# Kernel optimization log

Hardware: AMD Instinct MI355X
Metric: run time of the kernel (lower is better)

## Reference

```python
import jax, jax.numpy as jnp
import numpy as np

N_EDGES = 4096
HIDDEN = 256
EDGE_DIM = 128
NUM_HEADS = 4
NUM_GRAPHS = 64


def setup_inputs() -> dict:
    key0 = jax.random.key(0)
    ks = jax.random.split(key0, 10)
    s = 0.02
    inp = {
        "query": jax.random.normal(ks[0], (N_EDGES, HIDDEN), jnp.float32),
        "key": jax.random.normal(ks[1], (N_EDGES, EDGE_DIM), jnp.float32),
        "value": jax.random.normal(ks[2], (N_EDGES, EDGE_DIM), jnp.float32),
        "edge_graph_index": jnp.sort(
            jax.random.randint(ks[3], (N_EDGES,), 0, NUM_GRAPHS)
        ),
        # edge_proj: Linear(edge_context_dim -> hidden_dim)
        "w_edge": jax.random.normal(ks[4], (HIDDEN, EDGE_DIM), jnp.float32) * s,
        "b_edge": jnp.zeros((HIDDEN,), jnp.float32),
        # nn.MultiheadAttention packed in-projection [3H, H] and bias [3H]
        "w_in": jax.random.normal(ks[5], (3 * HIDDEN, HIDDEN), jnp.float32) * s,
        "b_in": jnp.zeros((3 * HIDDEN,), jnp.float32),
        # out_proj: Linear(hidden -> hidden)
        "w_out": jax.random.normal(ks[6], (HIDDEN, HIDDEN), jnp.float32) * s,
        "b_out": jnp.zeros((HIDDEN,), jnp.float32),
    }
    return inp


def reference(query, key, value, edge_graph_index,
              w_edge, b_edge, w_in, b_in, w_out, b_out):
    # Segment-wise cross attention == block-diagonal masked attention over all edges.
    N, H = query.shape
    nh = NUM_HEADS
    dh = H // nh

    # edge feature projection (applied to both key and value, as in the module)
    K = key @ w_edge.T + b_edge      # [N, H]
    V = value @ w_edge.T + b_edge    # [N, H]

    wq, wk, wv = jnp.split(w_in, 3, axis=0)
    bq, bk, bv = jnp.split(b_in, 3)
    Qh = (query @ wq.T + bq).reshape(N, nh, dh)
    Kh = (K @ wk.T + bk).reshape(N, nh, dh)
    Vh = (V @ wv.T + bv).reshape(N, nh, dh)

    scale = 1.0 / jnp.sqrt(jnp.asarray(dh, query.dtype))
    scores = jnp.einsum("nhd,mhd->hnm", Qh, Kh) * scale  # [nh, N, N]

    # attention only within the same graph segment
    same_graph = edge_graph_index[:, None] == edge_graph_index[None, :]  # [N, N]
    neg = jnp.finfo(scores.dtype).min
    scores = jnp.where(same_graph[None, :, :], scores, neg)

    attn = jax.nn.softmax(scores, axis=-1)                 # [nh, N, N]
    out = jnp.einsum("hnm,mhd->nhd", attn, Vh).reshape(N, H)
    out = out @ w_out.T + b_out
    return query + out
```

## Files before the change

kernel.cpp:

```cpp
#include <hip/hip_runtime.h>

#define N_EDGES 4096
#define HIDDEN  256
#define EDGE_DIM 128
#define NUM_HEADS 4
#define NUM_GRAPHS 64
#define DH 64

typedef __attribute__((ext_vector_type(8))) short short8;
typedef __attribute__((ext_vector_type(4))) float f32x4;

__device__ __forceinline__ unsigned short f2bf(float f) {
  unsigned u = __builtin_bit_cast(unsigned, f);
  u += 0x7FFF + ((u >> 16) & 1);
  return (unsigned short)(u >> 16);
}
__device__ __forceinline__ float bf2f(unsigned short u) {
  return __builtin_bit_cast(float, (unsigned)u << 16);
}
__device__ __forceinline__ short8 cvt8(float4 x, float4 y) {
  short8 v;
  v[0] = (short)f2bf(x.x); v[1] = (short)f2bf(x.y);
  v[2] = (short)f2bf(x.z); v[3] = (short)f2bf(x.w);
  v[4] = (short)f2bf(y.x); v[5] = (short)f2bf(y.y);
  v[6] = (short)f2bf(y.z); v[7] = (short)f2bf(y.w);
  return v;
}
__device__ __forceinline__ float4 us4f(ushort4 v) {
  float4 f;
  f.x = bf2f(v.x); f.y = bf2f(v.y); f.z = bf2f(v.z); f.w = bf2f(v.w);
  return f;
}

__device__ __forceinline__ int lbound(const int* __restrict__ a, int n, int v) {
  int lo = 0, hi = n;
  while (lo < hi) { int mid = (lo + hi) >> 1; if (a[mid] < v) lo = mid + 1; else hi = mid; }
  return lo;
}

template<bool ABF, bool OUTF32>
__device__ __forceinline__ void gemm_core(const void* Ap, const float* W,
                                          const float* bias, const float* res,
                                          void* Cp, const int K) {
  const int t = threadIdx.x;
  const int m0 = blockIdx.x * 64, n0 = blockIdx.y * 64;
  __shared__ unsigned short As[64 * 40];
  __shared__ unsigned short Ws[64 * 40];
  const int r = t >> 2, kg = t & 3;
  const int lane = t & 63, w = t >> 6;
  const int quad = lane >> 4, l16 = lane & 15;
  const int wm = (w >> 1) * 32, wn = (w & 1) * 32;
  f32x4 acc[2][2] = {};
  const float* pw = W + (size_t)(n0 + r) * K + kg * 8;
  float4 w0 = *(const float4*)(pw), w1 = *(const float4*)(pw + 4);
  const unsigned short* pa16 = (const unsigned short*)Ap + (size_t)(m0 + r) * K + kg * 8;
  const float* pa32 = (const float*)Ap + (size_t)(m0 + r) * K + kg * 8;
  short8 a16; float4 a0, a1;
  if (ABF) a16 = *(const short8*)pa16;
  else { a0 = *(const float4*)pa32; a1 = *(const float4*)(pa32 + 4); }
  for (int kc = 0; kc < K; kc += 32) {
    short8 na16; float4 na0, na1, nw0, nw1;
    if (kc + 32 < K) {
      if (ABF) na16 = *(const short8*)(pa16 + kc + 32);
      else { na0 = *(const float4*)(pa32 + kc + 32); na1 = *(const float4*)(pa32 + kc + 36); }
      nw0 = *(const float4*)(pw + kc + 32); nw1 = *(const float4*)(pw + kc + 36);
    }
    __syncthreads();
    short8 av = ABF ? a16 : cvt8(a0, a1);
    *(short8*)&As[r * 40 + kg * 8] = av;
    *(short8*)&Ws[r * 40 + kg * 8] = cvt8(w0, w1);
    __syncthreads();
    short8 af0 = *(const short8*)&As[(wm + l16) * 40 + quad * 8];
    short8 af1 = *(const short8*)&As[(wm + 16 + l16) * 40 + quad * 8];
    short8 bf0 = *(const short8*)&Ws[(wn + l16) * 40 + quad * 8];
    short8 bf1 = *(const short8*)&Ws[(wn + 16 + l16) * 40 + quad * 8];
    acc[0][0] = __builtin_amdgcn_mfma_f32_16x16x32_bf16(af0, bf0, acc[0][0], 0, 0, 0);
    acc[0][1] = __builtin_amdgcn_mfma_f32_16x16x32_bf16(af0, bf1, acc[0][1], 0, 0, 0);
    acc[1][0] = __builtin_amdgcn_mfma_f32_16x16x32_bf16(af1, bf0, acc[1][0], 0, 0, 0);
    acc[1][1] = __builtin_amdgcn_mfma_f32_16x16x32_bf16(af1, bf1, acc[1][1], 0, 0, 0);
    a16 = na16; a0 = na0; a1 = na1; w0 = nw0; w1 = nw1;
  }
#pragma unroll
  for (int j = 0; j < 2; ++j) {
    const int col = n0 + wn + j * 16 + l16;
    const float bj = bias[col];
#pragma unroll
    for (int i = 0; i < 2; ++i) {
#pragma unroll
      for (int reg = 0; reg < 4; ++reg) {
        const int row = m0 + wm + i * 16 + quad * 4 + reg;
        const size_t idx = (size_t)row * HIDDEN + col;
        float v = acc[i][j][reg] + bj;
        if (OUTF32) ((float*)Cp)[idx] = v + res[idx];
        else        ((unsigned short*)Cp)[idx] = f2bf(v);
      }
    }
  }
}

__global__ __launch_bounds__(256) void proj1(const float* __restrict__ query,
                                             const float* __restrict__ key,
                                             const float* __restrict__ value,
                                             const float* __restrict__ w_in,
                                             const float* __restrict__ b_in,
                                             const float* __restrict__ w_edge,
                                             const float* __restrict__ b_edge,
                                             const int* __restrict__ gidx,
                                             unsigned short* Qh, unsigned short* Ek,
                                             unsigned short* Ev, int* segStart) {
  if (blockIdx.z == 0 && blockIdx.x == 0 && blockIdx.y == 0 && threadIdx.x <= NUM_GRAPHS)
    segStart[threadIdx.x] = lbound(gidx, N_EDGES, threadIdx.x);
  if (blockIdx.z == 0)      gemm_core<false, false>(query, w_in,   b_in,   nullptr, Qh, 256);
  else if (blockIdx.z == 1) gemm_core<false, false>(key,   w_edge, b_edge, nullptr, Ek, 128);
  else                      gemm_core<false, false>(value, w_edge, b_edge, nullptr, Ev, 128);
}

__global__ __launch_bounds__(256) void proj2(const unsigned short* __restrict__ Ek,
                                             const unsigned short* __restrict__ Ev,
                                             const float* __restrict__ w_in,
                                             const float* __restrict__ b_in,
                                             unsigned short* Kh, unsigned short* Vh) {
  if (blockIdx.z == 0) gemm_core<true, false>(Ek, w_in + 256 * HIDDEN, b_in + 256, nullptr, Kh, 256);
  else                 gemm_core<true, false>(Ev, w_in + 512 * HIDDEN, b_in + 512, nullptr, Vh, 256);
}

__global__ __launch_bounds__(256) void attn_segment(const unsigned short* __restrict__ Qh,
                                                    const unsigned short* __restrict__ Kh,
                                                    const unsigned short* __restrict__ Vh,
                                                    const int* __restrict__ segStart,
                                                    unsigned short* __restrict__ ao) {
  const int graph = blockIdx.x, h = blockIdx.y, zg = blockIdx.z;
  const int segLo = segStart[graph];
  const int segHi = segStart[graph + 1];
  const int segLen = segHi - segLo;
  const int t = threadIdx.x, lane = t & 63, w = t >> 6;
  __shared__ float Qs[16][68], Ks[64][68], Vs[64][68];
  __shared__ float Ps[4][64][4];
  const float scale = 0.125f;
  const int r0 = w * 4;

  for (int chunk = zg; chunk * 16 < segLen; chunk += 8) {
    const int row0 = segLo + chunk * 16;
    const int rows = min(16, segHi - row0);
    __syncthreads();
    { int r = t >> 4, d4 = (t & 15) * 4;
      if (r < rows)
        *(float4*)&Qs[r][d4] =
            us4f(*(const ushort4*)(Qh + (size_t)(row0 + r) * HIDDEN + h * DH + d4)); }

    float accv[4] = {0.f, 0.f, 0.f, 0.f}, lsum[4] = {0.f, 0.f, 0.f, 0.f};

    for (int c0 = segLo; c0 < segHi; c0 += 64) {
      const int tc = min(64, segHi - c0);
      __syncthreads();
#pragma unroll
      for (int it = 0; it < 4; ++it) {
        int s = t + it * 256; int j = s >> 4; int d4 = (s & 15) * 4;
        if (j < tc) {
          *(float4*)&Ks[j][d4] =
              us4f(*(const ushort4*)(Kh + (size_t)(c0 + j) * HIDDEN + h * DH + d4));
          *(float4*)&Vs[j][d4] =
              us4f(*(const ushort4*)(Vh + (size_t)(c0 + j) * HIDDEN + h * DH + d4));
        }
      }
      __syncthreads();
      float4 kreg[16];
#pragma unroll
      for (int d4 = 0; d4 < 16; ++d4) kreg[d4] = *(const float4*)&Ks[lane][d4 * 4];
      float p[4];
#pragma unroll
      for (int r = 0; r < 4; ++r) {
        float s = 0.f;
#pragma unroll
        for (int d4 = 0; d4 < 16; ++d4) {
          float4 q = *(const float4*)&Qs[r0 + r][d4 * 4];
          s += q.x * kreg[d4].x + q.y * kreg[d4].y + q.z * kreg[d4].z + q.w * kreg[d4].w;
        }
        p[r] = (lane < tc && r0 + r < rows) ? __expf(s * scale) : 0.f;
        lsum[r] += p[r];
      }
      float4 p4; p4.x = p[0]; p4.y = p[1]; p4.z = p[2]; p4.w = p[3];
      *(float4*)&Ps[w][lane][0] = p4;
      __asm__ volatile("s_waitcnt lgkmcnt(0)" ::: "memory");
      for (int j = 0; j < tc; ++j) {
        const float v = Vs[j][lane];
        float4 pj = *(const float4*)&Ps[w][j][0];
        accv[0] += pj.x * v; accv[1] += pj.y * v;
        accv[2] += pj.z * v; accv[3] += pj.w * v;
      }
    }
#pragma unroll
    for (int off = 32; off; off >>= 1)
#pragma unroll
      for (int r = 0; r < 4; ++r) lsum[r] += __shfl_xor(lsum[r], off);
#pragma unroll
    for (int r = 0; r < 4; ++r)
      if (r0 + r < rows)
        ao[(size_t)(row0 + r0 + r) * HIDDEN + h * DH + lane] = f2bf(accv[r] / lsum[r]);
  }
}

__global__ __launch_bounds__(256) void outproj(const unsigned short* __restrict__ ao,
                                               const float* __restrict__ w_out,
                                               const float* __restrict__ b_out,
                                               const float* __restrict__ query,
                                               float* __restrict__ out) {
  gemm_core<true, true>(ao, w_out, b_out, query, out, 256);
}

extern "C" void kernel_launch(void* const* d_in, const int* in_sizes, int n_in,
                              void* d_out, int out_size, void* d_ws, size_t ws_size,
                              hipStream_t stream) {
  const float* query  = (const float*)d_in[0];
  const float* key    = (const float*)d_in[1];
  const float* value  = (const float*)d_in[2];
  const int*   gidx   = (const int*)d_in[3];
  const float* w_edge = (const float*)d_in[4];
  const float* b_edge = (const float*)d_in[5];
  const float* w_in   = (const float*)d_in[6];
  const float* b_in   = (const float*)d_in[7];
  const float* w_out  = (const float*)d_in[8];
  const float* b_out  = (const float*)d_in[9];
  float* out = (float*)d_out;

  int* segStart = (int*)d_ws;
  unsigned short* Qh = (unsigned short*)((char*)d_ws + 512);
  unsigned short* Ek = Qh + (size_t)N_EDGES * HIDDEN;
  unsigned short* Ev = Ek + (size_t)N_EDGES * HIDDEN;
  unsigned short* Kh = Ev + (size_t)N_EDGES * HIDDEN;
  unsigned short* Vh = Kh + (size_t)N_EDGES * HIDDEN;
  unsigned short* ao = Vh + (size_t)N_EDGES * HIDDEN;

  proj1<<<dim3(64, 4, 3), 256, 0, stream>>>(query, key, value, w_in, b_in,
                                            w_edge, b_edge, gidx, Qh, Ek, Ev, segStart);
  proj2<<<dim3(64, 4, 2), 256, 0, stream>>>(Ek, Ev, w_in, b_in, Kh, Vh);
  attn_segment<<<dim3(NUM_GRAPHS, NUM_HEADS, 8), 256, 0, stream>>>(Qh, Kh, Vh, segStart, ao);
  outproj<<<dim3(64, 4), 256, 0, stream>>>(ao, w_out, b_out, query, out);
}
```

Measured before the change: 117.7 us.

## Fold edge projection into K/V weights and fuse attention with output projection

Precomputes fused weights (w_in_k/v times w_edge) and biases in a small kernel, so key/value projection becomes one GEMM instead of two chained GEMMs with bf16 intermediates. Attention now loops over all heads inside a block and immediately applies the output projection plus residual using MFMA, eliminating the separate outproj kernel and the attention output buffer. This reduces launches and global traffic but cuts attention grid parallelism by the head count and reloads w_out from global per row chunk. Segment bounds are computed per block by binary search instead of a prepass.

```diff
diff --git a/kernel.cpp b/kernel.cpp
--- a/kernel.cpp
+++ b/kernel.cpp
@@ -38,174 +38,265 @@
   return lo;
 }
 
-template<bool ABF, bool OUTF32>
-__device__ __forceinline__ void gemm_core(const void* Ap, const float* W,
-                                          const float* bias, const float* res,
-                                          void* Cp, const int K) {
+template<bool WBF>
+__device__ __forceinline__ void gemm_tile(const float* __restrict__ Ap, const void* Wp,
+                                          const float* __restrict__ bias,
+                                          unsigned short* __restrict__ Cp, const int K,
+                                          const int m0, const int n0,
+                                          unsigned short* As, unsigned short* Ws) {
   const int t = threadIdx.x;
-  const int m0 = blockIdx.x * 64, n0 = blockIdx.y * 64;
-  __shared__ unsigned short As[64 * 40];
-  __shared__ unsigned short Ws[64 * 40];
   const int r = t >> 2, kg = t & 3;
   const int lane = t & 63, w = t >> 6;
   const int quad = lane >> 4, l16 = lane & 15;
   const int wm = (w >> 1) * 32, wn = (w & 1) * 32;
   f32x4 acc[2][2] = {};
-  const float* pw = W + (size_t)(n0 + r) * K + kg * 8;
-  float4 w0 = *(const float4*)(pw), w1 = *(const float4*)(pw + 4);
-  const unsigned short* pa16 = (const unsigned short*)Ap + (size_t)(m0 + r) * K + kg * 8;
-  const float* pa32 = (const float*)Ap + (size_t)(m0 + r) * K + kg * 8;
-  short8 a16; float4 a0, a1;
-  if (ABF) a16 = *(const short8*)pa16;
-  else { a0 = *(const float4*)pa32; a1 = *(const float4*)(pa32 + 4); }
+  const float* pa32 = Ap + (size_t)(m0 + r) * K + kg * 8;
+  const float*          pw32 = (const float*)Wp          + (size_t)(n0 + r) * K + kg * 8;
+  const unsigned short* pw16 = (const unsigned short*)Wp + (size_t)(n0 + r) * K + kg * 8;
+  short8 w16; float4 a0, a1, w0, w1;
+  a0 = *(const float4*)pa32; a1 = *(const float4*)(pa32 + 4);
+  if (WBF) w16 = *(const short8*)pw16;
+  else { w0 = *(const float4*)pw32; w1 = *(const float4*)(pw32 + 4); }
   for (int kc = 0; kc < K; kc += 32) {
-    short8 na16; float4 na0, na1, nw0, nw1;
+    short8 nw16; float4 na0, na1, nw0, nw1;
     if (kc + 32 < K) {
-      if (ABF) na16 = *(const short8*)(pa16 + kc + 32);
-      else { na0 = *(const float4*)(pa32 + kc + 32); na1 = *(const float4*)(pa32 + kc + 36); }
-      nw0 = *(const float4*)(pw + kc + 32); nw1 = *(const float4*)(pw + kc + 36);
+      na0 = *(const float4*)(pa32 + kc + 32); na1 = *(const float4*)(pa32 + kc + 36);
+      if (WBF) nw16 = *(const short8*)(pw16 + kc + 32);
+      else { nw0 = *(const float4*)(pw32 + kc + 32); nw1 = *(const float4*)(pw32 + kc + 36); }
     }
     __syncthreads();
-    short8 av = ABF ? a16 : cvt8(a0, a1);
-    *(short8*)&As[r * 40 + kg * 8] = av;
-    *(short8*)&Ws[r * 40 + kg * 8] = cvt8(w0, w1);
+    *(short8*)&As[r * 40 + kg * 8] = cvt8(a0, a1);
+    *(short8*)&Ws[r * 40 + kg * 8] = WBF ? w16 : cvt8(w0, w1);
     __syncthreads();
     short8 af0 = *(const short8*)&As[(wm + l16) * 40 + quad * 8];
     short8 af1 = *(const short8*)&As[(wm + 16 + l16) * 40 + quad * 8];
-    short8 bf0 = *(const short8*)&Ws[(wn + l16) * 40 + quad * 8];
-    short8 bf1 = *(const short8*)&Ws[(wn + 16 + l16) * 40 + quad * 8];
-    acc[0][0] = __builtin_amdgcn_mfma_f32_16x16x32_bf16(af0, bf0, acc[0][0], 0, 0, 0);
-    acc[0][1] = __builtin_amdgcn_mfma_f32_16x16x32_bf16(af0, bf1, acc[0][1], 0, 0, 0);
-    acc[1][0] = __builtin_amdgcn_mfma_f32_16x16x32_bf16(af1, bf0, acc[1][0], 0, 0, 0);
-    acc[1][1] = __builtin_amdgcn_mfma_f32_16x16x32_bf16(af1, bf1, acc[1][1], 0, 0, 0);
-    a16 = na16; a0 = na0; a1 = na1; w0 = nw0; w1 = nw1;
+    short8 bq0 = *(const short8*)&Ws[(wn + l16) * 40 + quad * 8];
+    short8 bq1 = *(const short8*)&Ws[(wn + 16 + l16) * 40 + quad * 8];
+    acc[0][0] = __builtin_amdgcn_mfma_f32_16x16x32_bf16(af0, bq0, acc[0][0], 0, 0, 0);
+    acc[0][1] = __builtin_amdgcn_mfma_f32_16x16x32_bf16(af0, bq1, acc[0][1], 0, 0, 0);
+    acc[1][0] = __builtin_amdgcn_mfma_f32_16x16x32_bf16(af1, bq0, acc[1][0], 0, 0, 0);
+    acc[1][1] = __builtin_amdgcn_mfma_f32_16x16x32_bf16(af1, bq1, acc[1][1], 0, 0, 0);
+    a0 = na0; a1 = na1; w16 = nw16; w0 = nw0; w1 = nw1;
   }
 #pragma unroll
   for (int j = 0; j < 2; ++j) {
     const int col = n0 + wn + j * 16 + l16;
     const float bj = bias[col];
 #pragma unroll
-    for (int i = 0; i < 2; ++i) {
+    for (int i = 0; i < 2; ++i)
 #pragma unroll
       for (int reg = 0; reg < 4; ++reg) {
         const int row = m0 + wm + i * 16 + quad * 4 + reg;
-        const size_t idx = (size_t)row * HIDDEN + col;
-        float v = acc[i][j][reg] + bj;
-        if (OUTF32) ((float*)Cp)[idx] = v + res[idx];
-        else        ((unsigned short*)Cp)[idx] = f2bf(v);
-      }
+        Cp[(size_t)row * HIDDEN + col] = f2bf(acc[i][j][reg] + bj);
+      }
+  }
+}
+
+__device__ __forceinline__ void wf_part(int bb, const float* __restrict__ w_in,
+                                        const float* __restrict__ b_in,
+                                        const float* __restrict__ w_edge,
+                                        const float* __restrict__ b_edge,
+                                        unsigned short* __restrict__ Wfk,
+                                        unsigned short* __restrict__ Wfv,
+                                        float* __restrict__ bfk, float* __restrict__ bfv,
+                                        unsigned short* As, unsigned short* Bs) {
+  const int sel = bb >> 3;
+  const int tt  = bb & 7;
+  const int n0  = (tt >> 1) * 64;
+  const int k0  = (tt & 1) * 64;
+  const float* Wp = w_in + (size_t)(256 + 256 * sel) * HIDDEN;
+  const float* bp = b_in + 256 + 256 * sel;
+  unsigned short* Wf = sel ? Wfv : Wfk;
+  float* bf = sel ? bfv : bfk;
+  const int t = threadIdx.x;
+  const int r = t >> 2, kg = t & 3;
+  const int lane = t & 63, w = t >> 6;
+  const int quad = lane >> 4, l16 = lane & 15;
+  const int wm = (w >> 1) * 32, wn = (w & 1) * 32;
+  if (k0 == 0) {
+    float s = 0.f;
+    const float* wrow = Wp + (size_t)(n0 + r) * HIDDEN + kg * 64;
+    const float* be = b_edge + kg * 64;
+#pragma unroll
+    for (int j = 0; j < 64; j += 4) {
+      float4 a = *(const float4*)(wrow + j);
+      float4 b = *(const float4*)(be + j);
+      s += a.x * b.x + a.y * b.y + a.z * b.z + a.w * b.w;
     }
-  }
-}
-
-__global__ __launch_bounds__(256) void proj1(const float* __restrict__ query,
-                                             const float* __restrict__ key,
-                                             const float* __restrict__ value,
-                                             const float* __restrict__ w_in,
-                                             const float* __restrict__ b_in,
-                                             const float* __restrict__ w_edge,
-                                             const float* __restrict__ b_edge,
-                                             const int* __restrict__ gidx,
-                                             unsigned short* Qh, unsigned short* Ek,
-                                             unsigned short* Ev, int* segStart) {
-  if (blockIdx.z == 0 && blockIdx.x == 0 && blockIdx.y == 0 && threadIdx.x <= NUM_GRAPHS)
-    segStart[threadIdx.x] = lbound(gidx, N_EDGES, threadIdx.x);
-  if (blockIdx.z == 0)      gemm_core<false, false>(query, w_in,   b_in,   nullptr, Qh, 256);
-  else if (blockIdx.z == 1) gemm_core<false, false>(key,   w_edge, b_edge, nullptr, Ek, 128);
-  else                      gemm_core<false, false>(value, w_edge, b_edge, nullptr, Ev, 128);
-}
-
-__global__ __launch_bounds__(256) void proj2(const unsigned short* __restrict__ Ek,
-                                             const unsigned short* __restrict__ Ev,
-                                             const float* __restrict__ w_in,
-                                             const float* __restrict__ b_in,
-                                             unsigned short* Kh, unsigned short* Vh) {
-  if (blockIdx.z == 0) gemm_core<true, false>(Ek, w_in + 256 * HIDDEN, b_in + 256, nullptr, Kh, 256);
-  else                 gemm_core<true, false>(Ev, w_in + 512 * HIDDEN, b_in + 512, nullptr, Vh, 256);
-}
-
-__global__ __launch_bounds__(256) void attn_segment(const unsigned short* __restrict__ Qh,
-                                                    const unsigned short* __restrict__ Kh,
-                                                    const unsigned short* __restrict__ Vh,
-                                                    const int* __restrict__ segStart,
-                                                    unsigned short* __restrict__ ao) {
-  const int graph = blockIdx.x, h = blockIdx.y, zg = blockIdx.z;
-  const int segLo = segStart[graph];
-  const int segHi = segStart[graph + 1];
+    s += __shfl_xor(s, 1); s += __shfl_xor(s, 2);
+    if (kg == 0) bf[n0 + r] = s + bp[n0 + r];
+  }
+  f32x4 facc[2][2] = {};
+  for (int j0 = 0; j0 < HIDDEN; j0 += 32) {
+    __syncthreads();
+    { const float* p = Wp + (size_t)(n0 + r) * HIDDEN + j0 + kg * 8;
+      float4 x0 = *(const float4*)p, x1 = *(const float4*)(p + 4);
+      *(short8*)&As[r * 40 + kg * 8] = cvt8(x0, x1); }
+    { const int j = t >> 3, k8 = (t & 7) * 8;
+      const float* p = w_edge + (size_t)(j0 + j) * EDGE_DIM + k0 + k8;
+      float4 b0 = *(const float4*)p, b1 = *(const float4*)(p + 4);
+      float bv[8] = {b0.x, b0.y, b0.z, b0.w, b1.x, b1.y, b1.z, b1.w};
+#pragma unroll
+      for (int i = 0; i < 8; ++i) Bs[(k8 + i) * 40 + j] = f2bf(bv[i]); }
+    __syncthreads();
+    short8 af0 = *(const short8*)&As[(wm + l16) * 40 + quad * 8];
+    short8 af1 = *(const short8*)&As[(wm + 16 + l16) * 40 + quad * 8];
+    short8 bq0 = *(const short8*)&Bs[(wn + l16) * 40 + quad * 8];
+    short8 bq1 = *(const short8*)&Bs[(wn + 16 + l16) * 40 + quad * 8];
+    facc[0][0] = __builtin_amdgcn_mfma_f32_16x16x32_bf16(af0, bq0, facc[0][0], 0, 0, 0);
+    facc[0][1] = __builtin_amdgcn_mfma_f32_16x16x32_bf16(af0, bq1, facc[0][1], 0, 0, 0);
+    facc[1][0] = __builtin_amdgcn_mfma_f32_16x16x32_bf16(af1, bq0, facc[1][0], 0, 0, 0);
+    facc[1][1] = __builtin_amdgcn_mfma_f32_16x16x32_bf16(af1, bq1, facc[1][1], 0, 0, 0);
+  }
+#pragma unroll
+  for (int jj = 0; jj < 2; ++jj)
+#pragma unroll
+    for (int ii = 0; ii < 2; ++ii)
+#pragma unroll
+      for (int reg = 0; reg < 4; ++reg) {
+        const int n = wm + ii * 16 + quad * 4 + reg;
+        const int k = wn + jj * 16 + l16;
+        Wf[(size_t)(n0 + n) * EDGE_DIM + k0 + k] = f2bf(facc[ii][jj][reg]);
+      }
+}
+
+__global__ __launch_bounds__(256) void k_wf(const float* __restrict__ w_in,
+                                            const float* __restrict__ b_in,
+                                            const float* __restrict__ w_edge,
+                                            const float* __restrict__ b_edge,
+                                            unsigned short* Wfk, unsigned short* Wfv,
+                                            float* bfk, float* bfv) {
+  __shared__ unsigned short As[64 * 40];
+  __shared__ unsigned short Bs[64 * 40];
+  wf_part(blockIdx.x, w_in, b_in, w_edge, b_edge, Wfk, Wfv, bfk, bfv, As, Bs);
+}
+
+__global__ __launch_bounds__(256) void k_proj(const float* __restrict__ query,
+                                              const float* __restrict__ key,
+                                              const float* __restrict__ value,
+                                              const float* __restrict__ w_in,
+                                              const float* __restrict__ b_in,
+                                              const unsigned short* __restrict__ Wfk,
+                                              const unsigned short* __restrict__ Wfv,
+                                              const float* __restrict__ bfk,
+                                              const float* __restrict__ bfv,
+                                              unsigned short* Qh, unsigned short* Kh,
+                                              unsigned short* Vh) {
+  __shared__ unsigned short As[64 * 40];
+  __shared__ unsigned short Ws[64 * 40];
+  const int m0 = blockIdx.x * 64, n0 = blockIdx.y * 64;
+  if (blockIdx.z == 0)      gemm_tile<false>(query, w_in, b_in, Qh, 256, m0, n0, As, Ws);
+  else if (blockIdx.z == 1) gemm_tile<true>(key, Wfk, bfk, Kh, 128, m0, n0, As, Ws);
+  else                      gemm_tile<true>(value, Wfv, bfv, Vh, 128, m0, n0, As, Ws);
+}
+
+__global__ __launch_bounds__(256) void k_attn_out(const unsigned short* __restrict__ Qh,
+                                                  const unsigned short* __restrict__ Kh,
+                                                  const unsigned short* __restrict__ Vh,
+                                                  const int* __restrict__ gidx,
+                                                  const float* __restrict__ w_out,
+                                                  const float* __restrict__ b_out,
+                                                  const float* __restrict__ query,
+                                                  float* __restrict__ out) {
+  const int g = blockIdx.x, ci = blockIdx.y;
+  const int segLo = lbound(gidx, N_EDGES, g);
+  const int segHi = lbound(gidx, N_EDGES, g + 1);
   const int segLen = segHi - segLo;
   const int t = threadIdx.x, lane = t & 63, w = t >> 6;
+  const int quad = lane >> 4, l16 = lane & 15;
   __shared__ float Qs[16][68], Ks[64][68], Vs[64][68];
   __shared__ float Ps[4][64][4];
+  __shared__ unsigned short aohS[16][264];
   const float scale = 0.125f;
   const int r0 = w * 4;
 
-  for (int chunk = zg; chunk * 16 < segLen; chunk += 8) {
+  for (int chunk = ci; chunk * 16 < segLen; chunk += 8) {
     const int row0 = segLo + chunk * 16;
     const int rows = min(16, segHi - row0);
-    __syncthreads();
-    { int r = t >> 4, d4 = (t & 15) * 4;
-      if (r < rows)
-        *(float4*)&Qs[r][d4] =
-            us4f(*(const ushort4*)(Qh + (size_t)(row0 + r) * HIDDEN + h * DH + d4)); }
-
-    float accv[4] = {0.f, 0.f, 0.f, 0.f}, lsum[4] = {0.f, 0.f, 0.f, 0.f};
-
-    for (int c0 = segLo; c0 < segHi; c0 += 64) {
-      const int tc = min(64, segHi - c0);
+
+    for (int h = 0; h < NUM_HEADS; ++h) {
       __syncthreads();
-#pragma unroll
-      for (int it = 0; it < 4; ++it) {
-        int s = t + it * 256; int j = s >> 4; int d4 = (s & 15) * 4;
-        if (j < tc) {
-          *(float4*)&Ks[j][d4] =
-              us4f(*(const ushort4*)(Kh + (size_t)(c0 + j) * HIDDEN + h * DH + d4));
-          *(float4*)&Vs[j][d4] =
-              us4f(*(const ushort4*)(Vh + (size_t)(c0 + j) * HIDDEN + h * DH + d4));
+      { int r = t >> 4, d4 = (t & 15) * 4;
+        if (r < rows)
+          *(float4*)&Qs[r][d4] =
+              us4f(*(const ushort4*)(Qh + (size_t)(row0 + r) * HIDDEN + h * DH + d4)); }
+
+      float accv[4] = {0.f, 0.f, 0.f, 0.f}, lsum[4] = {0.f, 0.f, 0.f, 0.f};
+
+      for (int c0 = segLo; c0 < segHi; c0 += 64) {
+        const int tc = min(64, segHi - c0);
+        __syncthreads();
+#pragma unroll
+        for (int it = 0; it < 4; ++it) {
+          int s = t + it * 256; int j = s >> 4; int d4 = (s & 15) * 4;
+          if (j < tc) {
+            *(float4*)&Ks[j][d4] =
+                us4f(*(const ushort4*)(Kh + (size_t)(c0 + j) * HIDDEN + h * DH + d4));
+            *(float4*)&Vs[j][d4] =
+                us4f(*(const ushort4*)(Vh + (size_t)(c0 + j) * HIDDEN + h * DH + d4));
+          }
         }
-      }
-      __syncthreads();
-      float4 kreg[16];
-#pragma unroll
-      for (int d4 = 0; d4 < 16; ++d4) kreg[d4] = *(const float4*)&Ks[lane][d4 * 4];
-      float p[4];
-#pragma unroll
-      for (int r = 0; r < 4; ++r) {
-        float s = 0.f;
-#pragma unroll
-        for (int d4 = 0; d4 < 16; ++d4) {
-          float4 q = *(const float4*)&Qs[r0 + r][d4 * 4];
-          s += q.x * kreg[d4].x + q.y * kreg[d4].y + q.z * kreg[d4].z + q.w * kreg[d4].w;
+        __syncthreads();
+        float4 kreg[16];
+#pragma unroll
+        for (int d4 = 0; d4 < 16; ++d4) kreg[d4] = *(const float4*)&Ks[lane][d4 * 4];
+        float p[4];
+#pragma unroll
+        for (int r = 0; r < 4; ++r) {
+          float s = 0.f;
+#pragma unroll
+          for (int d4 = 0; d4 < 16; ++d4) {
+            float4 q = *(const float4*)&Qs[r0 + r][d4 * 4];
+            s += q.x * kreg[d4].x + q.y * kreg[d4].y + q.z * kreg[d4].z + q.w * kreg[d4].w;
+          }
+          p[r] = (lane < tc && r0 + r < rows) ? __expf(s * scale) : 0.f;
+          lsum[r] += p[r];
         }
-        p[r] = (lane < tc && r0 + r < rows) ? __expf(s * scale) : 0.f;
-        lsum[r] += p[r];
-      }
-      float4 p4; p4.x = p[0]; p4.y = p[1]; p4.z = p[2]; p4.w = p[3];
-      *(float4*)&Ps[w][lane][0] = p4;
-      __asm__ volatile("s_waitcnt lgkmcnt(0)" ::: "memory");
-      for (int j = 0; j < tc; ++j) {
-        const float v = Vs[j][lane];
-        float4 pj = *(const float4*)&Ps[w][j][0];
-        accv[0] += pj.x * v; accv[1] += pj.y * v;
-        accv[2] += pj.z * v; accv[3] += pj.w * v;
-      }
+        float4 p4; p4.x = p[0]; p4.y = p[1]; p4.z = p[2]; p4.w = p[3];
+        *(float4*)&Ps[w][lane][0] = p4;
+        __asm__ volatile("s_waitcnt lgkmcnt(0)" ::: "memory");
+        for (int j = 0; j < tc; ++j) {
+          const float v = Vs[j][lane];
+          float4 pj = *(const float4*)&Ps[w][j][0];
+          accv[0] += pj.x * v; accv[1] += pj.y * v;
+          accv[2] += pj.z * v; accv[3] += pj.w * v;
+        }
+      }
+#pragma unroll
+      for (int off = 32; off; off >>= 1)
+#pragma unroll
+        for (int r = 0; r < 4; ++r) lsum[r] += __shfl_xor(lsum[r], off);
+#pragma unroll
+      for (int r = 0; r < 4; ++r)
+        aohS[r0 + r][h * DH + lane] =
+            (r0 + r < rows) ? f2bf(accv[r] / lsum[r]) : (unsigned short)0;
     }
-#pragma unroll
-    for (int off = 32; off; off >>= 1)
-#pragma unroll
-      for (int r = 0; r < 4; ++r) lsum[r] += __shfl_xor(lsum[r], off);
-#pragma unroll
-    for (int r = 0; r < 4; ++r)
-      if (r0 + r < rows)
-        ao[(size_t)(row0 + r0 + r) * HIDDEN + h * DH + lane] = f2bf(accv[r] / lsum[r]);
-  }
-}
-
-__global__ __launch_bounds__(256) void outproj(const unsigned short* __restrict__ ao,
-                                               const float* __restrict__ w_out,
-                                               const float* __restrict__ b_out,
-                                               const float* __restrict__ query,
-                                               float* __restrict__ out) {
-  gemm_core<true, true>(ao, w_out, b_out, query, out, 256);
+    __syncthreads();
+
+    f32x4 po[4] = {};
+#pragma unroll
+    for (int kc = 0; kc < HIDDEN; kc += 32) {
+      short8 af = *(const short8*)&aohS[l16][kc + quad * 8];
+#pragma unroll
+      for (int nt = 0; nt < 4; ++nt) {
+        const int n = w * 64 + nt * 16 + l16;
+        const float* p = w_out + (size_t)n * HIDDEN + kc + quad * 8;
+        float4 b0 = *(const float4*)p, b1 = *(const float4*)(p + 4);
+        po[nt] = __builtin_amdgcn_mfma_f32_16x16x32_bf16(af, cvt8(b0, b1), po[nt], 0, 0, 0);
+      }
+    }
+#pragma unroll
+    for (int nt = 0; nt < 4; ++nt)
+#pragma unroll
+      for (int reg = 0; reg < 4; ++reg) {
+        const int rr = quad * 4 + reg;
+        const int col = w * 64 + nt * 16 + l16;
+        if (rr < rows) {
+          const size_t idx = (size_t)(row0 + rr) * HIDDEN + col;
+          out[idx] = po[nt][reg] + b_out[col] + query[idx];
+        }
+      }
+  }
 }
 
 extern "C" void kernel_launch(void* const* d_in, const int* in_sizes, int n_in,
@@ -223,17 +314,17 @@
   const float* b_out  = (const float*)d_in[9];
   float* out = (float*)d_out;
 
-  int* segStart = (int*)d_ws;
-  unsigned short* Qh = (unsigned short*)((char*)d_ws + 512);
-  unsigned short* Ek = Qh + (size_t)N_EDGES * HIDDEN;
-  unsigned short* Ev = Ek + (size_t)N_EDGES * HIDDEN;
-  unsigned short* Kh = Ev + (size_t)N_EDGES * HIDDEN;
-  unsigned short* Vh = Kh + (size_t)N_EDGES * HIDDEN;
-  unsigned short* ao = Vh + (size_t)N_EDGES * HIDDEN;
-
-  proj1<<<dim3(64, 4, 3), 256, 0, stream>>>(query, key, value, w_in, b_in,
-                                            w_edge, b_edge, gidx, Qh, Ek, Ev, segStart);
-  proj2<<<dim3(64, 4, 2), 256, 0, stream>>>(Ek, Ev, w_in, b_in, Kh, Vh);
-  attn_segment<<<dim3(NUM_GRAPHS, NUM_HEADS, 8), 256, 0, stream>>>(Qh, Kh, Vh, segStart, ao);
-  outproj<<<dim3(64, 4), 256, 0, stream>>>(ao, w_out, b_out, query, out);
-}
+  unsigned short* Qh  = (unsigned short*)d_ws;
+  unsigned short* Kh  = Qh + (size_t)N_EDGES * HIDDEN;
+  unsigned short* Vh  = Kh + (size_t)N_EDGES * HIDDEN;
+  unsigned short* Wfk = Vh + (size_t)N_EDGES * HIDDEN;
+  unsigned short* Wfv = Wfk + 256 * EDGE_DIM;
+  float* bfk = (float*)(Wfv + 256 * EDGE_DIM);
+  float* bfv = bfk + 256;
+
+  k_wf<<<dim3(16), 256, 0, stream>>>(w_in, b_in, w_edge, b_edge, Wfk, Wfv, bfk, bfv);
+  k_proj<<<dim3(64, 4, 3), 256, 0, stream>>>(query, key, value, w_in, b_in,
+                                             Wfk, Wfv, bfk, bfv, Qh, Kh, Vh);
+  k_attn_out<<<dim3(NUM_GRAPHS, 8), 256, 0, stream>>>(Qh, Kh, Vh, gidx,
+                                                      w_out, b_out, query, out);
+}
```

New measurement: 156.7 us. 1.33x slower.
